# Optimization experiments

Measured on AMD Instinct MI355X. Metric: run time of the kernel, lower is better.

The kernel has to match this reference:

```python
import jax, jax.numpy as jnp
import numpy as np

V, N, H = 4, 4096, 128
EDGE_P = 0.002  # sparsity of generated adjacency


def setup_inputs() -> dict:
    key = jax.random.key(0)
    ks = jax.random.split(key, 12)
    # binary adjacency, zero diagonal (dense_to_sparse treats nonzeros as edges)
    adjs = (jax.random.uniform(ks[0], (V, N, N)) < EDGE_P).astype(jnp.float32)
    idx = jnp.arange(N)
    adjs = adjs.at[:, idx, idx].set(0.0)
    s = 0.05
    return {
        "adjs": adjs,
        "w1": jax.random.normal(ks[1], (V, N, H), jnp.float32) * s,
        "b1": jnp.zeros((V, H), jnp.float32),
        "w2": jax.random.normal(ks[2], (V, H, H), jnp.float32) * s,
        "b2": jnp.zeros((V, H), jnp.float32),
        "wa1": jax.random.normal(ks[3], (H, 64), jnp.float32) * s,
        "ba1": jnp.zeros((64,), jnp.float32),
        "wa2": jax.random.normal(ks[4], (64,), jnp.float32) * s,
        "ba2": jnp.zeros((1,), jnp.float32),
        "wf1": jax.random.normal(ks[5], (V * H, 2 * H), jnp.float32) * s,
        "bf1": jnp.zeros((2 * H,), jnp.float32),
        "wf2": jax.random.normal(ks[6], (2 * H, 128), jnp.float32) * s,
        "bf2": jnp.zeros((128,), jnp.float32),
    }


def _gcn_norm(adjs):
    # GCNConv default: A_hat = A + I, A_norm = D^-1/2 A_hat D^-1/2 (edge weight 1)
    n = adjs.shape[-1]
    idx = jnp.arange(n)
    a_hat = (adjs != 0).astype(adjs.dtype).at[:, idx, idx].set(1.0)
    dinv = jax.lax.rsqrt(a_hat.sum(-1))  # [V,N], deg>=1 due to self loops
    return dinv[:, :, None] * a_hat * dinv[:, None, :]


def reference(adjs, w1, b1, w2, b2, wa1, ba1, wa2, ba2, wf1, bf1, wf2, bf2):
    a_norm = _gcn_norm(adjs)  # [V,N,N]
    # initial features X = I_N, so X @ w1 == w1; dropout is inference no-op
    h1 = jax.nn.relu(jnp.einsum('vij,vjh->vih', a_norm, w1) + b1[:, None, :])
    h2 = jax.nn.relu(
        jnp.einsum('vij,vjh->vih', a_norm, jnp.einsum('vnh,vhk->vnk', h1, w2))
        + b2[:, None, :])  # [V,N,H] per-view embeddings
    # attention fusion
    summaries = h2.mean(axis=1)  # [V,H]
    scores = jnp.tanh(summaries @ wa1 + ba1) @ wa2 + ba2[0]  # [V]
    attn = jax.nn.softmax(scores, axis=0)  # [V]
    weighted = h2 * attn[:, None, None]  # [V,N,H]
    fusion_in = jnp.transpose(weighted, (1, 0, 2)).reshape(weighted.shape[1], -1)  # [N, V*H]
    fused = jax.nn.relu(fusion_in @ wf1 + bf1) @ wf2 + bf2  # [N, fusion_out]
    return fused, attn, h2
```

## Files before the change

kernel.cpp:

```cpp
#include <hip/hip_runtime.h>

#define VV 4
#define NN 4096
#define HH 128
#define CAP 64
#define R2 16
#define FR 16
#define CHP (NN / R2)

typedef __attribute__((ext_vector_type(4))) float fvec4;

__global__ __launch_bounds__(256) void k_build_csr(
    const float* __restrict__ adjs, int* __restrict__ nbr,
    int* __restrict__ cnt, float* __restrict__ dinv)
{
    int wave = threadIdx.x >> 6;
    int lane = threadIdx.x & 63;
    int r = blockIdx.x * 4 + wave;
    const fvec4* row = (const fvec4*)(adjs + (size_t)r * NN);
    int* out = nbr + (size_t)r * CAP;
    unsigned long long lm = (1ull << lane) - 1ull;
    int base = 0;
    #pragma unroll 4
    for (int c = 0; c < NN / 256; ++c) {
        fvec4 x = __builtin_nontemporal_load(&row[c * 64 + lane]);
        int c0 = (x.x != 0.f), c1 = (x.y != 0.f), c2 = (x.z != 0.f), c3 = (x.w != 0.f);
        unsigned long long b0 = __ballot(c0), b1 = __ballot(c1);
        unsigned long long b2 = __ballot(c2), b3 = __ballot(c3);
        int pos = base + __popcll(b0 & lm) + __popcll(b1 & lm)
                       + __popcll(b2 & lm) + __popcll(b3 & lm);
        int e = c * 256 + lane * 4;
        if (c0 && pos < CAP) out[pos] = e;     pos += c0;
        if (c1 && pos < CAP) out[pos] = e + 1; pos += c1;
        if (c2 && pos < CAP) out[pos] = e + 2; pos += c2;
        if (c3 && pos < CAP) out[pos] = e + 3; pos += c3;
        base += __popcll(b0) + __popcll(b1) + __popcll(b2) + __popcll(b3);
    }
    if (lane == 0) {
        cnt[r]  = base < CAP ? base : CAP;
        dinv[r] = rsqrtf((float)(base + 1));
    }
}

__global__ __launch_bounds__(512) void k_spmm1(
    const float* __restrict__ w1, const float* __restrict__ b1,
    const int* __restrict__ nbr, const int* __restrict__ cnt,
    const float* __restrict__ dinv, float* __restrict__ h1)
{
    int xcd  = blockIdx.x & 7;
    int slot = blockIdx.x >> 3;
    int wid  = (xcd >> 1) * 1024 + slot * 2 + (xcd & 1);
    int g = threadIdx.x >> 7;
    int h = threadIdx.x & 127;
    int r = wid * 4 + g;
    int v = r >> 12;
    __shared__ int   s_j[4][CAP];
    __shared__ float s_w[4][CAP];
    int n = cnt[r];
    float dr = dinv[r];
    if (h < n) {
        int j = nbr[(size_t)r * CAP + h];
        s_j[g][h] = j;
        s_w[g][h] = dinv[v * NN + j];
    }
    __syncthreads();
    float acc = dr * w1[(size_t)r * HH + h];
    #pragma unroll 4
    for (int k = 0; k < n; ++k)
        acc += s_w[g][k] * w1[((size_t)(v * NN + s_j[g][k])) * HH + h];
    float val = dr * acc + b1[v * HH + h];
    h1[(size_t)r * HH + h] = val > 0.f ? val : 0.f;
}

__global__ __launch_bounds__(256) void k_layer2(
    const float* __restrict__ h1, const float* __restrict__ w2,
    const float* __restrict__ b2, const int* __restrict__ nbr,
    const int* __restrict__ cnt, const float* __restrict__ dinv,
    float* __restrict__ h2, float* __restrict__ part)
{
    int xcd  = blockIdx.x & 7;
    int slot = blockIdx.x >> 3;
    int wid  = (xcd >> 1) * 256 + slot * 2 + (xcd & 1);
    int v   = wid >> 8;
    int gr0 = wid * R2;
    __shared__ int   s_n[R2];
    __shared__ float s_dr[R2];
    __shared__ int   s_j[R2][CAP];
    __shared__ float s_w[R2][CAP];
    __shared__ float s_u[R2][HH];
    __shared__ float s_p[8][HH];

    if (threadIdx.x < R2) {
        s_n[threadIdx.x]  = cnt[gr0 + threadIdx.x];
        s_dr[threadIdx.x] = dinv[gr0 + threadIdx.x];
    }
    __syncthreads();
    for (int idx = threadIdx.x; idx < R2 * CAP; idx += 256) {
        int rr = idx >> 6, kk = idx & 63;
        if (kk < s_n[rr]) {
            int j = nbr[(size_t)(gr0 + rr) * CAP + kk];
            s_j[rr][kk] = j;
            s_w[rr][kk] = dinv[v * NN + j];
        }
    }
    __syncthreads();

    {
        int rr  = threadIdx.x >> 4;
        int t16 = threadIdx.x & 15;
        int h0  = t16 * 8;
        int n   = s_n[rr];
        float dr = s_dr[rr];
        const float* self = h1 + (size_t)(gr0 + rr) * HH + h0;
        float a[8];
        #pragma unroll
        for (int q = 0; q < 8; ++q) a[q] = dr * self[q];
        #pragma unroll 4
        for (int k = 0; k < n; ++k) {
            float wj = s_w[rr][k];
            const float4* src = (const float4*)(h1 + ((size_t)(v * NN + s_j[rr][k])) * HH + h0);
            float4 x0 = src[0], x1 = src[1];
            a[0] += wj * x0.x; a[1] += wj * x0.y; a[2] += wj * x0.z; a[3] += wj * x0.w;
            a[4] += wj * x1.x; a[5] += wj * x1.y; a[6] += wj * x1.z; a[7] += wj * x1.w;
        }
        float4 o0 = { dr * a[0], dr * a[1], dr * a[2], dr * a[3] };
        float4 o1 = { dr * a[4], dr * a[5], dr * a[6], dr * a[7] };
        *(float4*)&s_u[rr][h0]     = o0;
        *(float4*)&s_u[rr][h0 + 4] = o1;
    }
    __syncthreads();

    int r0 = (threadIdx.x >> 5) * 2;
    int c0 = (threadIdx.x & 31) * 4;
    const float* wv = w2 + (size_t)v * HH * HH;
    float acc[2][4];
    #pragma unroll
    for (int i = 0; i < 2; ++i)
        #pragma unroll
        for (int j = 0; j < 4; ++j) acc[i][j] = 0.f;
    for (int k = 0; k < HH; k += 4) {
        float4 a[2], w[4];
        #pragma unroll
        for (int i = 0; i < 2; ++i) a[i] = *(const float4*)&s_u[r0 + i][k];
        #pragma unroll
        for (int kk = 0; kk < 4; ++kk) w[kk] = *(const float4*)&wv[(size_t)(k + kk) * HH + c0];
        #pragma unroll
        for (int i = 0; i < 2; ++i)
            #pragma unroll
            for (int j = 0; j < 4; ++j) {
                acc[i][j] += a[i].x * ((const float*)&w[0])[j];
                acc[i][j] += a[i].y * ((const float*)&w[1])[j];
                acc[i][j] += a[i].z * ((const float*)&w[2])[j];
                acc[i][j] += a[i].w * ((const float*)&w[3])[j];
            }
    }
    float p[4];
    #pragma unroll
    for (int j = 0; j < 4; ++j) {
        float b = b2[v * HH + c0 + j];
        float v0 = acc[0][j] + b, v1 = acc[1][j] + b;
        v0 = v0 > 0.f ? v0 : 0.f;
        v1 = v1 > 0.f ? v1 : 0.f;
        acc[0][j] = v0; acc[1][j] = v1;
        p[j] = v0 + v1;
    }
    #pragma unroll
    for (int i = 0; i < 2; ++i) {
        float4 o = { acc[i][0], acc[i][1], acc[i][2], acc[i][3] };
        *(float4*)&h2[(size_t)(gr0 + r0 + i) * HH + c0] = o;
    }
    *(float4*)&s_p[threadIdx.x >> 5][c0] = *(float4*)p;
    __syncthreads();
    if (threadIdx.x < HH) {
        float a = 0.f;
        #pragma unroll
        for (int q = 0; q < 8; ++q) a += s_p[q][threadIdx.x];
        part[(size_t)wid * HH + threadIdx.x] = a;
    }
}

__global__ __launch_bounds__(512) void k_attn(
    const float* __restrict__ part, const float* __restrict__ wa1,
    const float* __restrict__ ba1, const float* __restrict__ wa2,
    const float* __restrict__ ba2, float* __restrict__ attn_out,
    float* __restrict__ attn_ws)
{
    __shared__ float s_sum[VV * HH];
    __shared__ float s_red[256];
    __shared__ float s_score[VV];
    {
        int v = threadIdx.x >> 7, h = threadIdx.x & 127;
        float a = 0.f;
        #pragma unroll 8
        for (int c = 0; c < CHP; ++c) a += part[(size_t)(v * CHP + c) * HH + h];
        s_sum[v * HH + h] = a * (1.0f / NN);
    }
    __syncthreads();
    if (threadIdx.x < 256) {
        int v = threadIdx.x >> 6, u = threadIdx.x & 63;
        float a = ba1[u];
        for (int k = 0; k < HH; ++k) a += s_sum[v * HH + k] * wa1[k * 64 + u];
        s_red[threadIdx.x] = tanhf(a) * wa2[u];
    }
    __syncthreads();
    if (threadIdx.x < VV) {
        float sc = ba2[0];
        for (int uu = 0; uu < 64; ++uu) sc += s_red[threadIdx.x * 64 + uu];
        s_score[threadIdx.x] = sc;
    }
    __syncthreads();
    if (threadIdx.x == 0) {
        float m = s_score[0];
        for (int i = 1; i < VV; ++i) m = fmaxf(m, s_score[i]);
        float e[VV], den = 0.f;
        for (int i = 0; i < VV; ++i) { e[i] = __expf(s_score[i] - m); den += e[i]; }
        for (int i = 0; i < VV; ++i) {
            float av = e[i] / den;
            attn_out[i] = av;
            attn_ws[i]  = av;
        }
    }
}

#define S1 516
#define S2 260
#define S3 132
__global__ __launch_bounds__(512) void k_fusion(
    const float* __restrict__ h2, const float* __restrict__ attn_ws,
    const float* __restrict__ wf1, const float* __restrict__ bf1,
    const float* __restrict__ wf2, const float* __restrict__ bf2,
    float* __restrict__ fused)
{
    __shared__ float s_in[FR][S1];
    __shared__ float s_hid[FR][S2];
    float (*s_part)[S2] = (float (*)[S2])&s_in[0][0];
    float (*s_p2)[S3]   = (float (*)[S3])&s_in[0][0];

    int nbase = blockIdx.x * FR;
    int wv   = threadIdx.x >> 6;
    int lane = threadIdx.x & 63;
    float at[VV];
    #pragma unroll
    for (int v = 0; v < VV; ++v) at[v] = attn_ws[v];

    for (int idx = threadIdx.x; idx < FR * 128; idx += 512) {
        int r  = idx >> 7;
        int c4 = idx & 127;
        int v  = c4 >> 5;
        int h4 = c4 & 31;
        const float4* srcr = (const float4*)(h2 + ((size_t)v * NN + nbase + r) * HH);
        float4 x = srcr[h4];
        float s = at[v];
        x.x *= s; x.y *= s; x.z *= s; x.w *= s;
        *(float4*)&s_in[r][c4 * 4] = x;
    }
    __syncthreads();

    int cg = wv & 3, kh = wv >> 2;
    int ccol  = cg * 64 + (lane & 15) * 4;
    int rbase = (lane >> 4) * 4;
    float acc[4][4];
    #pragma unroll
    for (int i = 0; i < 4; ++i)
        #pragma unroll
        for (int j = 0; j < 4; ++j) acc[i][j] = 0.f;
    {
        int k0 = kh * 256;
        const float* wrow = wf1 + (size_t)k0 * 256 + ccol;
        #pragma unroll 4
        for (int k = 0; k < 256; ++k) {
            float4 wk = *(const float4*)wrow;
            wrow += 256;
            float a0 = s_in[rbase + 0][k0 + k];
            float a1 = s_in[rbase + 1][k0 + k];
            float a2 = s_in[rbase + 2][k0 + k];
            float a3 = s_in[rbase + 3][k0 + k];
            acc[0][0] += a0 * wk.x; acc[0][1] += a0 * wk.y; acc[0][2] += a0 * wk.z; acc[0][3] += a0 * wk.w;
            acc[1][0] += a1 * wk.x; acc[1][1] += a1 * wk.y; acc[1][2] += a1 * wk.z; acc[1][3] += a1 * wk.w;
            acc[2][0] += a2 * wk.x; acc[2][1] += a2 * wk.y; acc[2][2] += a2 * wk.z; acc[2][3] += a2 * wk.w;
            acc[3][0] += a3 * wk.x; acc[3][1] += a3 * wk.y; acc[3][2] += a3 * wk.z; acc[3][3] += a3 * wk.w;
        }
    }
    __syncthreads();
    if (kh == 1) {
        #pragma unroll
        for (int i = 0; i < 4; ++i)
            *(float4*)&s_part[rbase + i][ccol] = *(float4*)&acc[i][0];
    }
    __syncthreads();
    if (kh == 0) {
        float4 b = *(const float4*)&bf1[ccol];
        #pragma unroll
        for (int i = 0; i < 4; ++i) {
            float4 p = *(float4*)&s_part[rbase + i][ccol];
            float h0 = acc[i][0] + p.x + b.x;
            float h1v = acc[i][1] + p.y + b.y;
            float h2v = acc[i][2] + p.z + b.z;
            float h3 = acc[i][3] + p.w + b.w;
            float4 o;
            o.x = h0 > 0.f ? h0 : 0.f;
            o.y = h1v > 0.f ? h1v : 0.f;
            o.z = h2v > 0.f ? h2v : 0.f;
            o.w = h3 > 0.f ? h3 : 0.f;
            *(float4*)&s_hid[rbase + i][ccol] = o;
        }
    }
    __syncthreads();

    int cg2 = wv & 3, kh2 = wv >> 2;
    int c2 = cg2 * 32 + (lane & 15) * 2;
    float acc2[4][2];
    #pragma unroll
    for (int i = 0; i < 4; ++i) { acc2[i][0] = 0.f; acc2[i][1] = 0.f; }
    {
        int k0 = kh2 * 128;
        const float* wrow = wf2 + (size_t)k0 * 128 + c2;
        #pragma unroll 4
        for (int k = 0; k < 128; ++k) {
            float2 wk = *(const float2*)wrow;
            wrow += 128;
            #pragma unroll
            for (int i = 0; i < 4; ++i) {
                float a = s_hid[rbase + i][k0 + k];
                acc2[i][0] += a * wk.x;
                acc2[i][1] += a * wk.y;
            }
        }
    }
    __syncthreads();
    if (kh2 == 1) {
        #pragma unroll
        for (int i = 0; i < 4; ++i) {
            float2 o = { acc2[i][0], acc2[i][1] };
            *(float2*)&s_p2[rbase + i][c2] = o;
        }
    }
    __syncthreads();
    if (kh2 == 0) {
        float b0 = bf2[c2], b1 = bf2[c2 + 1];
        #pragma unroll
        for (int i = 0; i < 4; ++i) {
            float2 p = *(float2*)&s_p2[rbase + i][c2];
            float2 o = { acc2[i][0] + p.x + b0, acc2[i][1] + p.y + b1 };
            *(float2*)&fused[(size_t)(nbase + rbase + i) * HH + c2] = o;
        }
    }
}

extern "C" void kernel_launch(void* const* d_in, const int* in_sizes, int n_in,
                              void* d_out, int out_size, void* d_ws, size_t ws_size,
                              hipStream_t stream)
{
    const float* adjs = (const float*)d_in[0];
    const float* w1   = (const float*)d_in[1];
    const float* b1   = (const float*)d_in[2];
    const float* w2   = (const float*)d_in[3];
    const float* b2   = (const float*)d_in[4];
    const float* wa1  = (const float*)d_in[5];
    const float* ba1  = (const float*)d_in[6];
    const float* wa2  = (const float*)d_in[7];
    const float* ba2  = (const float*)d_in[8];
    const float* wf1  = (const float*)d_in[9];
    const float* bf1  = (const float*)d_in[10];
    const float* wf2  = (const float*)d_in[11];
    const float* bf2  = (const float*)d_in[12];

    float* out   = (float*)d_out;
    float* fused = out;
    float* attn  = out + (size_t)NN * HH;
    float* h2    = attn + VV;

    char* w = (char*)d_ws;
    int*   nbr    = (int*)w;    w += (size_t)VV * NN * CAP * sizeof(int);
    int*   cnt    = (int*)w;    w += (size_t)VV * NN * sizeof(int);
    float* dinv   = (float*)w;  w += (size_t)VV * NN * sizeof(float);
    float* h1     = (float*)w;  w += (size_t)VV * NN * HH * sizeof(float);
    float* part   = (float*)w;  w += (size_t)VV * CHP * HH * sizeof(float);
    float* attnws = (float*)w;  w += 256;

    k_build_csr<<<VV * NN / 4, 256, 0, stream>>>(adjs, nbr, cnt, dinv);
    k_spmm1<<<VV * NN / 4, 512, 0, stream>>>(w1, b1, nbr, cnt, dinv, h1);
    k_layer2<<<VV * NN / R2, 256, 0, stream>>>(h1, w2, b2, nbr, cnt, dinv, h2, part);
    k_attn<<<1, 512, 0, stream>>>(part, wa1, ba1, wa2, ba2, attn, attnws);
    k_fusion<<<NN / FR, 512, 0, stream>>>(h2, attnws, wf1, bf1, wf2, bf2, fused);
}
```

Before: 134.9 us.

## Split layer-2 into separate gather and dense GEMM kernels, retile fusion

The fused layer-2 kernel, which gathered neighbour rows and then ran the 128x128 GEMM in one block, is split in two. A gather kernel in the same style as layer 1 writes the aggregated features u to a new workspace buffer, and a GEMM kernel then handles 32 rows per block with a 4x4 register tile. The fusion kernel's rows per block drop from 16 to 8 to give more blocks. This trades an extra global round trip of u (about 8 MB) and one more launch for better gather parallelism and more reuse in the GEMM.

Result: slower. 151.1 us (+12.0%).

```diff
diff --git a/kernel.cpp b/kernel.cpp
--- a/kernel.cpp
+++ b/kernel.cpp
@@ -4,9 +4,9 @@
 #define NN 4096
 #define HH 128
 #define CAP 64
-#define R2 16
-#define FR 16
-#define CHP (NN / R2)
+#define GR 32
+#define FR 8
+#define CHP (NN / GR)
 
 typedef __attribute__((ext_vector_type(4))) float fvec4;
 
@@ -72,80 +72,66 @@
     h1[(size_t)r * HH + h] = val > 0.f ? val : 0.f;
 }
 
-__global__ __launch_bounds__(256) void k_layer2(
-    const float* __restrict__ h1, const float* __restrict__ w2,
-    const float* __restrict__ b2, const int* __restrict__ nbr,
+__global__ __launch_bounds__(512) void k_gather2(
+    const float* __restrict__ h1, const int* __restrict__ nbr,
     const int* __restrict__ cnt, const float* __restrict__ dinv,
-    float* __restrict__ h2, float* __restrict__ part)
+    float* __restrict__ u)
 {
     int xcd  = blockIdx.x & 7;
     int slot = blockIdx.x >> 3;
-    int wid  = (xcd >> 1) * 256 + slot * 2 + (xcd & 1);
-    int v   = wid >> 8;
-    int gr0 = wid * R2;
-    __shared__ int   s_n[R2];
-    __shared__ float s_dr[R2];
-    __shared__ int   s_j[R2][CAP];
-    __shared__ float s_w[R2][CAP];
-    __shared__ float s_u[R2][HH];
+    int wid  = (xcd >> 1) * 1024 + slot * 2 + (xcd & 1);
+    int g = threadIdx.x >> 7;
+    int h = threadIdx.x & 127;
+    int r = wid * 4 + g;
+    int v = r >> 12;
+    __shared__ int   s_j[4][CAP];
+    __shared__ float s_w[4][CAP];
+    int n = cnt[r];
+    float dr = dinv[r];
+    if (h < n) {
+        int j = nbr[(size_t)r * CAP + h];
+        s_j[g][h] = j;
+        s_w[g][h] = dinv[v * NN + j];
+    }
+    __syncthreads();
+    float acc = dr * h1[(size_t)r * HH + h];
+    #pragma unroll 4
+    for (int k = 0; k < n; ++k)
+        acc += s_w[g][k] * h1[((size_t)(v * NN + s_j[g][k])) * HH + h];
+    u[(size_t)r * HH + h] = dr * acc;
+}
+
+__global__ __launch_bounds__(256) void k_gemm2c(
+    const float* __restrict__ u, const float* __restrict__ w2,
+    const float* __restrict__ b2, float* __restrict__ h2,
+    float* __restrict__ part)
+{
+    const int bpv = NN / GR;
+    int v = blockIdx.x / bpv;
+    int rbase_g = blockIdx.x * GR;
+    __shared__ float s_u[GR][HH];
     __shared__ float s_p[8][HH];
-
-    if (threadIdx.x < R2) {
-        s_n[threadIdx.x]  = cnt[gr0 + threadIdx.x];
-        s_dr[threadIdx.x] = dinv[gr0 + threadIdx.x];
-    }
-    __syncthreads();
-    for (int idx = threadIdx.x; idx < R2 * CAP; idx += 256) {
-        int rr = idx >> 6, kk = idx & 63;
-        if (kk < s_n[rr]) {
-            int j = nbr[(size_t)(gr0 + rr) * CAP + kk];
-            s_j[rr][kk] = j;
-            s_w[rr][kk] = dinv[v * NN + j];
-        }
-    }
-    __syncthreads();
-
-    {
-        int rr  = threadIdx.x >> 4;
-        int t16 = threadIdx.x & 15;
-        int h0  = t16 * 8;
-        int n   = s_n[rr];
-        float dr = s_dr[rr];
-        const float* self = h1 + (size_t)(gr0 + rr) * HH + h0;
-        float a[8];
-        #pragma unroll
-        for (int q = 0; q < 8; ++q) a[q] = dr * self[q];
-        #pragma unroll 4
-        for (int k = 0; k < n; ++k) {
-            float wj = s_w[rr][k];
-            const float4* src = (const float4*)(h1 + ((size_t)(v * NN + s_j[rr][k])) * HH + h0);
-            float4 x0 = src[0], x1 = src[1];
-            a[0] += wj * x0.x; a[1] += wj * x0.y; a[2] += wj * x0.z; a[3] += wj * x0.w;
-            a[4] += wj * x1.x; a[5] += wj * x1.y; a[6] += wj * x1.z; a[7] += wj * x1.w;
-        }
-        float4 o0 = { dr * a[0], dr * a[1], dr * a[2], dr * a[3] };
-        float4 o1 = { dr * a[4], dr * a[5], dr * a[6], dr * a[7] };
-        *(float4*)&s_u[rr][h0]     = o0;
-        *(float4*)&s_u[rr][h0 + 4] = o1;
-    }
-    __syncthreads();
-
-    int r0 = (threadIdx.x >> 5) * 2;
+    const float4* src = (const float4*)(u + (size_t)rbase_g * HH);
+    for (int idx = threadIdx.x; idx < GR * HH / 4; idx += 256)
+        ((float4*)s_u)[idx] = src[idx];
+    __syncthreads();
+
+    int r0 = (threadIdx.x >> 5) * 4;
     int c0 = (threadIdx.x & 31) * 4;
     const float* wv = w2 + (size_t)v * HH * HH;
-    float acc[2][4];
-    #pragma unroll
-    for (int i = 0; i < 2; ++i)
+    float acc[4][4];
+    #pragma unroll
+    for (int i = 0; i < 4; ++i)
         #pragma unroll
         for (int j = 0; j < 4; ++j) acc[i][j] = 0.f;
     for (int k = 0; k < HH; k += 4) {
-        float4 a[2], w[4];
-        #pragma unroll
-        for (int i = 0; i < 2; ++i) a[i] = *(const float4*)&s_u[r0 + i][k];
+        float4 a[4], w[4];
+        #pragma unroll
+        for (int i = 0; i < 4; ++i) a[i] = *(const float4*)&s_u[r0 + i][k];
         #pragma unroll
         for (int kk = 0; kk < 4; ++kk) w[kk] = *(const float4*)&wv[(size_t)(k + kk) * HH + c0];
         #pragma unroll
-        for (int i = 0; i < 2; ++i)
+        for (int i = 0; i < 4; ++i)
             #pragma unroll
             for (int j = 0; j < 4; ++j) {
                 acc[i][j] += a[i].x * ((const float*)&w[0])[j];
@@ -158,16 +144,21 @@
     #pragma unroll
     for (int j = 0; j < 4; ++j) {
         float b = b2[v * HH + c0 + j];
-        float v0 = acc[0][j] + b, v1 = acc[1][j] + b;
-        v0 = v0 > 0.f ? v0 : 0.f;
-        v1 = v1 > 0.f ? v1 : 0.f;
-        acc[0][j] = v0; acc[1][j] = v1;
-        p[j] = v0 + v1;
-    }
-    #pragma unroll
-    for (int i = 0; i < 2; ++i) {
+        float s = 0.f;
+        #pragma unroll
+        for (int i = 0; i < 4; ++i) {
+            float val = acc[i][j] + b;
+            val = val > 0.f ? val : 0.f;
+            acc[i][j] = val;
+            s += val;
+        }
+        p[j] = s;
+    }
+    float* dst = h2 + (size_t)rbase_g * HH;
+    #pragma unroll
+    for (int i = 0; i < 4; ++i) {
         float4 o = { acc[i][0], acc[i][1], acc[i][2], acc[i][3] };
-        *(float4*)&h2[(size_t)(gr0 + r0 + i) * HH + c0] = o;
+        *(float4*)&dst[(size_t)(r0 + i) * HH + c0] = o;
     }
     *(float4*)&s_p[threadIdx.x >> 5][c0] = *(float4*)p;
     __syncthreads();
@@ -175,7 +166,7 @@
         float a = 0.f;
         #pragma unroll
         for (int q = 0; q < 8; ++q) a += s_p[q][threadIdx.x];
-        part[(size_t)wid * HH + threadIdx.x] = a;
+        part[(size_t)blockIdx.x * HH + threadIdx.x] = a;
     }
 }
 
@@ -258,10 +249,10 @@
 
     int cg = wv & 3, kh = wv >> 2;
     int ccol  = cg * 64 + (lane & 15) * 4;
-    int rbase = (lane >> 4) * 4;
-    float acc[4][4];
-    #pragma unroll
-    for (int i = 0; i < 4; ++i)
+    int rbase = (lane >> 4) * 2;
+    float acc[2][4];
+    #pragma unroll
+    for (int i = 0; i < 2; ++i)
         #pragma unroll
         for (int j = 0; j < 4; ++j) acc[i][j] = 0.f;
     {
@@ -273,54 +264,49 @@
             wrow += 256;
             float a0 = s_in[rbase + 0][k0 + k];
             float a1 = s_in[rbase + 1][k0 + k];
-            float a2 = s_in[rbase + 2][k0 + k];
-            float a3 = s_in[rbase + 3][k0 + k];
             acc[0][0] += a0 * wk.x; acc[0][1] += a0 * wk.y; acc[0][2] += a0 * wk.z; acc[0][3] += a0 * wk.w;
             acc[1][0] += a1 * wk.x; acc[1][1] += a1 * wk.y; acc[1][2] += a1 * wk.z; acc[1][3] += a1 * wk.w;
-            acc[2][0] += a2 * wk.x; acc[2][1] += a2 * wk.y; acc[2][2] += a2 * wk.z; acc[2][3] += a2 * wk.w;
-            acc[3][0] += a3 * wk.x; acc[3][1] += a3 * wk.y; acc[3][2] += a3 * wk.z; acc[3][3] += a3 * wk.w;
         }
     }
     __syncthreads();
     if (kh == 1) {
         #pragma unroll
-        for (int i = 0; i < 4; ++i)
+        for (int i = 0; i < 2; ++i)
             *(float4*)&s_part[rbase + i][ccol] = *(float4*)&acc[i][0];
     }
     __syncthreads();
     if (kh == 0) {
         float4 b = *(const float4*)&bf1[ccol];
         #pragma unroll
-        for (int i = 0; i < 4; ++i) {
+        for (int i = 0; i < 2; ++i) {
             float4 p = *(float4*)&s_part[rbase + i][ccol];
-            float h0 = acc[i][0] + p.x + b.x;
+            float h0  = acc[i][0] + p.x + b.x;
             float h1v = acc[i][1] + p.y + b.y;
             float h2v = acc[i][2] + p.z + b.z;
-            float h3 = acc[i][3] + p.w + b.w;
+            float h3  = acc[i][3] + p.w + b.w;
             float4 o;
-            o.x = h0 > 0.f ? h0 : 0.f;
+            o.x = h0  > 0.f ? h0  : 0.f;
             o.y = h1v > 0.f ? h1v : 0.f;
             o.z = h2v > 0.f ? h2v : 0.f;
-            o.w = h3 > 0.f ? h3 : 0.f;
+            o.w = h3  > 0.f ? h3  : 0.f;
             *(float4*)&s_hid[rbase + i][ccol] = o;
         }
     }
     __syncthreads();
 
-    int cg2 = wv & 3, kh2 = wv >> 2;
-    int c2 = cg2 * 32 + (lane & 15) * 2;
-    float acc2[4][2];
-    #pragma unroll
-    for (int i = 0; i < 4; ++i) { acc2[i][0] = 0.f; acc2[i][1] = 0.f; }
+    int c2 = cg * 32 + (lane & 15) * 2;
+    float acc2[2][2];
+    #pragma unroll
+    for (int i = 0; i < 2; ++i) { acc2[i][0] = 0.f; acc2[i][1] = 0.f; }
     {
-        int k0 = kh2 * 128;
+        int k0 = kh * 128;
         const float* wrow = wf2 + (size_t)k0 * 128 + c2;
         #pragma unroll 4
         for (int k = 0; k < 128; ++k) {
             float2 wk = *(const float2*)wrow;
             wrow += 128;
             #pragma unroll
-            for (int i = 0; i < 4; ++i) {
+            for (int i = 0; i < 2; ++i) {
                 float a = s_hid[rbase + i][k0 + k];
                 acc2[i][0] += a * wk.x;
                 acc2[i][1] += a * wk.y;
@@ -328,18 +314,18 @@
         }
     }
     __syncthreads();
-    if (kh2 == 1) {
-        #pragma unroll
-        for (int i = 0; i < 4; ++i) {
+    if (kh == 1) {
+        #pragma unroll
+        for (int i = 0; i < 2; ++i) {
             float2 o = { acc2[i][0], acc2[i][1] };
             *(float2*)&s_p2[rbase + i][c2] = o;
         }
     }
     __syncthreads();
-    if (kh2 == 0) {
+    if (kh == 0) {
         float b0 = bf2[c2], b1 = bf2[c2 + 1];
         #pragma unroll
-        for (int i = 0; i < 4; ++i) {
+        for (int i = 0; i < 2; ++i) {
             float2 p = *(float2*)&s_p2[rbase + i][c2];
             float2 o = { acc2[i][0] + p.x + b0, acc2[i][1] + p.y + b1 };
             *(float2*)&fused[(size_t)(nbase + rbase + i) * HH + c2] = o;
@@ -375,12 +361,14 @@
     int*   cnt    = (int*)w;    w += (size_t)VV * NN * sizeof(int);
     float* dinv   = (float*)w;  w += (size_t)VV * NN * sizeof(float);
     float* h1     = (float*)w;  w += (size_t)VV * NN * HH * sizeof(float);
+    float* u      = (float*)w;  w += (size_t)VV * NN * HH * sizeof(float);
     float* part   = (float*)w;  w += (size_t)VV * CHP * HH * sizeof(float);
     float* attnws = (float*)w;  w += 256;
 
     k_build_csr<<<VV * NN / 4, 256, 0, stream>>>(adjs, nbr, cnt, dinv);
     k_spmm1<<<VV * NN / 4, 512, 0, stream>>>(w1, b1, nbr, cnt, dinv, h1);
-    k_layer2<<<VV * NN / R2, 256, 0, stream>>>(h1, w2, b2, nbr, cnt, dinv, h2, part);
+    k_gather2<<<VV * NN / 4, 512, 0, stream>>>(h1, nbr, cnt, dinv, u);
+    k_gemm2c<<<VV * NN / GR, 256, 0, stream>>>(u, w2, b2, h2, part);
     k_attn<<<1, 512, 0, stream>>>(part, wa1, ba1, wa2, ba2, attn, attnws);
     k_fusion<<<NN / FR, 512, 0, stream>>>(h2, attnws, wf1, bf1, wf2, bf2, fused);
 }
```
